# Kernel optimization log

Measured on AMD Instinct MI355X. Metric: run time of the kernel, lower is better.

## Reference

```python
import jax, jax.numpy as jnp
import numpy as np

EPS = 1e-5
QMAX = 127.0   # 8-bit symmetric: representable range [-128, 127]
QMIN = -128.0


def ste_round(x):
    # straight-through rounding (identity gradient)
    return x + jax.lax.stop_gradient(jnp.round(x) - x)


def setup_inputs() -> dict:
    key = jax.random.key(0)
    ks = jax.random.split(key, 7)
    N, C_in, C_out, H, W = 64, 256, 128, 56, 56
    x = jax.random.normal(ks[0], (N, C_in, H, W), jnp.float32)
    act_scaling_factor = jax.random.uniform(ks[1], (1,), jnp.float32, 0.02, 0.08)
    bn_weight = 1.0 + 0.3 * jax.random.normal(ks[2], (C_in,), jnp.float32)
    bn_bias = 0.1 * jax.random.normal(ks[3], (C_in,), jnp.float32)
    bn_mean = 0.1 * jax.random.normal(ks[4], (C_in,), jnp.float32)
    bn_var = jax.random.uniform(ks[5], (C_in,), jnp.float32, 0.5, 1.5)
    conv_weight = 0.05 * jax.random.normal(ks[6], (C_out, C_in, 1, 1), jnp.float32)
    return {
        "x": x,
        "act_scaling_factor": act_scaling_factor,
        "bn_weight": bn_weight,
        "bn_bias": bn_bias,
        "bn_mean": bn_mean,
        "bn_var": bn_var,
        "conv_weight": conv_weight,
    }


def _fwd(x, act_scaling_factor, bn_weight, bn_bias, bn_mean, bn_var, conv_weight):
    act_sf = act_scaling_factor.reshape(())

    # ---- QuantBn: fold BN, quantize folded scale per-channel (8-bit symmetric) ----
    inv_std = jax.lax.rsqrt(bn_var + EPS)
    scale = bn_weight * inv_std                    # [C_in]
    shift = bn_bias - bn_mean * scale              # [C_in]
    bn_sf = jnp.max(jnp.abs(scale)) / QMAX         # per-tensor bn weight scale
    scale_q = jnp.clip(ste_round(scale / bn_sf), QMIN, QMAX) * bn_sf
    bias_sf = bn_sf * act_sf                        # bias quantized at combined scale
    shift_q = ste_round(shift / bias_sf) * bias_sf
    x = x * scale_q[None, :, None, None] + shift_q[None, :, None, None]

    # ---- ReLU ----
    x = jnp.maximum(x, 0.0)

    # ---- QuantAct 1: per-tensor symmetric 8-bit requant ----
    sf1 = jnp.max(jnp.abs(x)) / QMAX
    x = jnp.clip(ste_round(x / sf1), QMIN, QMAX) * sf1

    # ---- QuantConv2d: per-output-channel 8-bit symmetric weight quant, 1x1 conv ----
    w_sf = jnp.max(jnp.abs(conv_weight), axis=(1, 2, 3)) / QMAX   # [C_out]
    w_q = jnp.clip(ste_round(conv_weight / w_sf[:, None, None, None]), QMIN, QMAX) \
          * w_sf[:, None, None, None]
    y = jax.lax.conv_general_dilated(
        x, w_q, window_strides=(1, 1), padding='VALID',
        dimension_numbers=('NCHW', 'OIHW', 'NCHW'))

    # ---- QuantAct 2 ----
    sf2 = jnp.max(jnp.abs(y)) / QMAX
    y = jnp.clip(ste_round(y / sf2), QMIN, QMAX) * sf2

    # ---- QuantAveragePool2d (2x2, stride 2): average in integer domain, re-round ----
    N, C, H, W = y.shape
    y_int = (y / sf2).reshape(N, C, H // 2, 2, W // 2, 2).mean(axis=(3, 5))
    out = ste_round(y_int) * sf2
    return out, sf2


def reference(x, act_scaling_factor, bn_weight, bn_bias, bn_mean, bn_var, conv_weight):
    return _fwd(x, act_scaling_factor, bn_weight, bn_bias, bn_mean, bn_var, conv_weight)
```

## Files before the change

kernel.cpp:

```cpp
#include <hip/hip_runtime.h>

#define QMAXF 127.0f
typedef int i32x4 __attribute__((ext_vector_type(4)));

__device__ __forceinline__ unsigned fkey(float f) {
  const unsigned b = __float_as_uint(f);
  return (b & 0x80000000u) ? ~b : (b | 0x80000000u);
}
__device__ __forceinline__ float fdec(unsigned u) {
  return __uint_as_float((u & 0x80000000u) ? (u & 0x7FFFFFFFu) : ~u);
}

__global__ __launch_bounds__(256) void k0_zero(unsigned* __restrict__ p) {
  const int t = threadIdx.x;
  p[t] = 0u; p[t + 256] = 0u; p[t + 512] = 0u; p[t + 768] = 0u;
}

__global__ __launch_bounds__(256, 8) void k1_minmax(
    const float* __restrict__ x, const float* __restrict__ actsf,
    const float* __restrict__ bnw, const float* __restrict__ bnb,
    const float* __restrict__ bnm, const float* __restrict__ bnv,
    const float* __restrict__ cw, unsigned* __restrict__ chanKmx,
    unsigned* __restrict__ chanKmn, float* __restrict__ scq,
    float* __restrict__ shq, float* __restrict__ wsf,
    signed char* __restrict__ wq8) {
  const int t = threadIdx.x, b = blockIdx.x;
  if (b == 2048) {
    __shared__ float red[4];
    float scale, shift;
    {
#pragma clang fp contract(off)
      float inv = 1.0f / sqrtf(bnv[t] + 1e-5f);
      scale = bnw[t] * inv;
      float tmp = bnm[t] * scale;
      shift = bnb[t] - tmp;
    }
    float a = fabsf(scale);
    for (int o = 32; o > 0; o >>= 1) a = fmaxf(a, __shfl_xor(a, o));
    if ((t & 63) == 0) red[t >> 6] = a;
    __syncthreads();
    const float amax = fmaxf(fmaxf(red[0], red[1]), fmaxf(red[2], red[3]));
    const float bn_sf = amax / QMAXF;
    scq[t] = fminf(fmaxf(rintf(scale / bn_sf), -128.f), 127.f) * bn_sf;
    const float bias_sf = bn_sf * actsf[0];
    shq[t] = rintf(shift / bias_sf) * bias_sf;
    const int r = t >> 1, half = t & 1;
    const float4* wrow = (const float4*)(cw + r * 256 + half * 128);
    float mx = 0.f;
#pragma unroll
    for (int j = 0; j < 32; ++j) {
      const float4 v = wrow[j];
      mx = fmaxf(mx, fmaxf(fmaxf(fabsf(v.x), fabsf(v.y)), fmaxf(fabsf(v.z), fabsf(v.w))));
    }
    mx = fmaxf(mx, __shfl_xor(mx, 1));
    const float wsf_v = mx / QMAXF;
    if (half == 0) wsf[r] = wsf_v;
    int* w8w = (int*)wq8;
#pragma unroll
    for (int j = 0; j < 32; ++j) {
      const float4 v = wrow[j];
      const float q0 = fminf(fmaxf(rintf(v.x / wsf_v), -128.f), 127.f);
      const float q1 = fminf(fmaxf(rintf(v.y / wsf_v), -128.f), 127.f);
      const float q2 = fminf(fmaxf(rintf(v.z / wsf_v), -128.f), 127.f);
      const float q3 = fminf(fmaxf(rintf(v.w / wsf_v), -128.f), 127.f);
      w8w[r * 64 + half * 32 + j] =
          ((int)q0 & 255) | (((int)q1 & 255) << 8) | (((int)q2 & 255) << 16) | (((int)q3 & 255) << 24);
    }
    return;
  }
  __shared__ float redmn[4][8], redmx[4][8];
  const int n = b >> 5, cg = b & 31;
  const float4* __restrict__ x4 = (const float4*)x + (long)(n * 256 + cg * 8) * 784;
  float mn[8], mx[8];
#pragma unroll
  for (int r = 0; r < 8; ++r) { mn[r] = __builtin_inff(); mx[r] = -__builtin_inff(); }
#pragma unroll
  for (int r = 0; r < 8; ++r) {
    const float4* row = x4 + r * 784;
    for (int j = t; j < 784; j += 256) {
      const float4 v = row[j];
      mn[r] = fminf(mn[r], fminf(fminf(v.x, v.y), fminf(v.z, v.w)));
      mx[r] = fmaxf(mx[r], fmaxf(fmaxf(v.x, v.y), fmaxf(v.z, v.w)));
    }
  }
#pragma unroll
  for (int r = 0; r < 8; ++r)
    for (int o = 32; o > 0; o >>= 1) {
      mn[r] = fminf(mn[r], __shfl_xor(mn[r], o));
      mx[r] = fmaxf(mx[r], __shfl_xor(mx[r], o));
    }
  if ((t & 63) == 0) {
#pragma unroll
    for (int r = 0; r < 8; ++r) { redmn[t >> 6][r] = mn[r]; redmx[t >> 6][r] = mx[r]; }
  }
  __syncthreads();
  if (t < 8) {
    const float fmn = fminf(fminf(redmn[0][t], redmn[1][t]), fminf(redmn[2][t], redmn[3][t]));
    const float fmx = fmaxf(fmaxf(redmx[0][t], redmx[1][t]), fmaxf(redmx[2][t], redmx[3][t]));
    atomicMax(&chanKmx[cg * 8 + t], fkey(fmx));
    atomicMax(&chanKmn[cg * 8 + t], ~fkey(fmn));
  }
}

__global__ __launch_bounds__(256, 4) void k2f_quant_gemm(
    const float* __restrict__ x, const float* __restrict__ scq,
    const float* __restrict__ shq, const unsigned* __restrict__ chanKmx,
    const unsigned* __restrict__ chanKmn, const signed char* __restrict__ wq8,
    const float* __restrict__ wsf, signed char* __restrict__ xqT,
    float* __restrict__ blockmax) {
  __shared__ __align__(16) unsigned char ldsb[112 * 256];
  __shared__ float s_scq[256], s_shq[256];
  __shared__ float comax[128];
  __shared__ float red[4];
  __shared__ float sf1s;
  const int t = threadIdx.x, w = t >> 6, l = t & 63, m = l & 15, g = l >> 4;
  const int blk = blockIdx.x, n = blk / 28, tt = blk - n * 28;

  {
    const float s = scq[t], sh = shq[t];
    s_scq[t] = s; s_shq[t] = sh;
    const float xe = (s >= 0.f) ? fdec(chanKmx[t]) : fdec(~chanKmn[t]);
    float z;
    {
#pragma clang fp contract(off)
      z = xe * s + sh;
    }
    float mm = fmaxf(z, 0.f);
    for (int o = 32; o > 0; o >>= 1) mm = fmaxf(mm, __shfl_xor(mm, o));
    if (l == 0) red[w] = mm;
    __syncthreads();
    if (t == 0) sf1s = fmaxf(fmaxf(red[0], red[1]), fmaxf(red[2], red[3])) / QMAXF;
    __syncthreads();
  }
  const float sf1 = sf1s;
  const float* __restrict__ xb = x + (long)n * 802816 + tt * 112;

  for (int it = 0; it < 28; ++it) {
    const int idx = it * 256 + t;
    const int c = idx / 28;
    const int p = idx - c * 28;
    const float4 v = *(const float4*)(xb + (long)c * 3136 + 4 * p);
    const float s = s_scq[c], sh = s_shq[c];
    float z0, z1, z2, z3;
    {
#pragma clang fp contract(off)
      z0 = v.x * s + sh; z1 = v.y * s + sh; z2 = v.z * s + sh; z3 = v.w * s + sh;
    }
    const float q0 = fminf(fmaxf(rintf(fmaxf(z0, 0.f) / sf1), -128.f), 127.f);
    const float q1 = fminf(fmaxf(rintf(fmaxf(z1, 0.f) / sf1), -128.f), 127.f);
    const float q2 = fminf(fmaxf(rintf(fmaxf(z2, 0.f) / sf1), -128.f), 127.f);
    const float q3 = fminf(fmaxf(rintf(fmaxf(z3, 0.f) / sf1), -128.f), 127.f);
    const int cs = c ^ ((p & 15) << 4);
    const int hw0 = 4 * p;
    ldsb[(hw0 + 0) * 256 + cs] = (unsigned char)((int)q0 & 255);
    ldsb[(hw0 + 1) * 256 + cs] = (unsigned char)((int)q1 & 255);
    ldsb[(hw0 + 2) * 256 + cs] = (unsigned char)((int)q2 & 255);
    ldsb[(hw0 + 3) * 256 + cs] = (unsigned char)((int)q3 & 255);
  }
  __syncthreads();

  signed char* __restrict__ dst = xqT + ((long)(n * 3136 + tt * 112)) * 256;
#pragma unroll
  for (int it = 0; it < 7; ++it) {
    const int idx = it * 256 + t;
    const int hw = idx >> 4, c16 = idx & 15;
    const i32x4 v = *(const i32x4*)&ldsb[hw * 256 + ((c16 * 16) ^ (((hw >> 2) & 15) << 4))];
    *(i32x4*)(dst + hw * 256 + c16 * 16) = v;
  }

  i32x4 acc[2][7];
#pragma unroll
  for (int ct = 0; ct < 2; ++ct)
#pragma unroll
    for (int ht = 0; ht < 7; ++ht) acc[ct][ht] = (i32x4){0, 0, 0, 0};
#pragma unroll
  for (int ks = 0; ks < 4; ++ks) {
    const i32x4 wf0 = *(const i32x4*)(wq8 + (w * 32 + m) * 256 + ks * 64 + g * 16);
    const i32x4 wf1 = *(const i32x4*)(wq8 + (w * 32 + 16 + m) * 256 + ks * 64 + g * 16);
#pragma unroll
    for (int ht = 0; ht < 7; ++ht) {
      const int row = ht * 16 + m;
      const i32x4 xf = *(const i32x4*)&ldsb[row * 256 +
                          ((ks * 64 + g * 16) ^ (((row >> 2) & 15) << 4))];
      acc[0][ht] = __builtin_amdgcn_mfma_i32_16x16x64_i8(wf0, xf, acc[0][ht], 0, 0, 0);
      acc[1][ht] = __builtin_amdgcn_mfma_i32_16x16x64_i8(wf1, xf, acc[1][ht], 0, 0, 0);
    }
  }

  int im[2][4];
#pragma unroll
  for (int ct = 0; ct < 2; ++ct)
#pragma unroll
    for (int r = 0; r < 4; ++r) {
      int v = 0;
#pragma unroll
      for (int ht = 0; ht < 7; ++ht) {
        int a = acc[ct][ht][r];
        a = a < 0 ? -a : a;
        v = a > v ? a : v;
      }
      im[ct][r] = v;
    }
#pragma unroll
  for (int o = 1; o < 16; o <<= 1)
#pragma unroll
    for (int ct = 0; ct < 2; ++ct)
#pragma unroll
      for (int r = 0; r < 4; ++r) {
        const int other = __shfl_xor(im[ct][r], o);
        im[ct][r] = other > im[ct][r] ? other : im[ct][r];
      }
  if (m == 0) {
#pragma unroll
    for (int ct = 0; ct < 2; ++ct)
#pragma unroll
      for (int r = 0; r < 4; ++r)
        comax[w * 32 + ct * 16 + g * 4 + r] = (float)im[ct][r];
  }
  __syncthreads();
  float v = 0.f;
  if (t < 128) v = comax[t] * (sf1 * wsf[t]);
  for (int o = 32; o > 0; o >>= 1) v = fmaxf(v, __shfl_xor(v, o));
  if (l == 0) red[w] = v;
  __syncthreads();
  if (t == 0)
    blockmax[blk] = fmaxf(fmaxf(red[0], red[1]), fmaxf(red[2], red[3]));
}

__global__ __launch_bounds__(256, 3) void k3_final(
    const signed char* __restrict__ xqT, const signed char* __restrict__ wq8,
    const float* __restrict__ wsf, const float* __restrict__ scq,
    const float* __restrict__ shq, const unsigned* __restrict__ chanKmx,
    const unsigned* __restrict__ chanKmn, const float* __restrict__ blockmax,
    float* __restrict__ out, float* __restrict__ outsf2) {
  __shared__ _Float16 q2[128 * 116];
  __shared__ float red[4];
  __shared__ float sf1s, sf2s;
  const int t = threadIdx.x, w = t >> 6, l = t & 63;
  const int m = l & 15, g = l >> 4;
  const int blk = blockIdx.x;
  const int n = blk / 28, tt = blk - n * 28;

  {
    const float s = scq[t], sh = shq[t];
    const float xe = (s >= 0.f) ? fdec(chanKmx[t]) : fdec(~chanKmn[t]);
    float z;
    {
#pragma clang fp contract(off)
      z = xe * s + sh;
    }
    float mm = fmaxf(z, 0.f);
    for (int o = 32; o > 0; o >>= 1) mm = fmaxf(mm, __shfl_xor(mm, o));
    if (l == 0) red[w] = mm;
    __syncthreads();
    if (t == 0) sf1s = fmaxf(fmaxf(red[0], red[1]), fmaxf(red[2], red[3])) / QMAXF;
  }
  {
    float bm = 0.f;
    for (int i = t; i < 1792; i += 256) bm = fmaxf(bm, blockmax[i]);
    for (int o = 32; o > 0; o >>= 1) bm = fmaxf(bm, __shfl_xor(bm, o));
    __syncthreads();
    if (l == 0) red[w] = bm;
    __syncthreads();
    if (t == 0) sf2s = fmaxf(fmaxf(red[0], red[1]), fmaxf(red[2], red[3])) / QMAXF;
    __syncthreads();
  }
  const float sf1 = sf1s;
  const float sf2 = sf2s;
  if (blk == 0 && t == 0) outsf2[0] = sf2;

  const signed char* __restrict__ xb = xqT + ((long)(n * 3136 + tt * 112)) * 256;
  i32x4 acc[2][7];
#pragma unroll
  for (int ct = 0; ct < 2; ++ct)
#pragma unroll
    for (int ht = 0; ht < 7; ++ht) acc[ct][ht] = (i32x4){0, 0, 0, 0};
#pragma unroll
  for (int ks = 0; ks < 4; ++ks) {
    const i32x4 wf0 = *(const i32x4*)(wq8 + (w * 32 + m) * 256 + ks * 64 + g * 16);
    const i32x4 wf1 = *(const i32x4*)(wq8 + (w * 32 + 16 + m) * 256 + ks * 64 + g * 16);
#pragma unroll
    for (int ht = 0; ht < 7; ++ht) {
      const i32x4 xf = *(const i32x4*)(xb + (ht * 16 + m) * 256 + ks * 64 + g * 16);
      acc[0][ht] = __builtin_amdgcn_mfma_i32_16x16x64_i8(wf0, xf, acc[0][ht], 0, 0, 0);
      acc[1][ht] = __builtin_amdgcn_mfma_i32_16x16x64_i8(wf1, xf, acc[1][ht], 0, 0, 0);
    }
  }
  float fac[2][4];
#pragma unroll
  for (int ct = 0; ct < 2; ++ct)
#pragma unroll
    for (int r = 0; r < 4; ++r)
      fac[ct][r] = sf1 * wsf[w * 32 + ct * 16 + g * 4 + r];
#pragma unroll
  for (int ct = 0; ct < 2; ++ct)
#pragma unroll
    for (int ht = 0; ht < 7; ++ht)
#pragma unroll
      for (int r = 0; r < 4; ++r) {
        const float y = (float)acc[ct][ht][r] * fac[ct][r];
        const float q = fminf(fmaxf(rintf(y / sf2), -128.f), 127.f);
        q2[(w * 32 + ct * 16 + g * 4 + r) * 116 + ht * 16 + m] = (_Float16)q;
      }
  __syncthreads();
  const long obase = (long)n * 100352 + tt * 28;
  for (int i = t; i < 3584; i += 256) {
    const unsigned co = (unsigned)i / 28u;
    const unsigned wo = (unsigned)i - co * 28u;
    const _Float16* row = q2 + co * 116;
    const float a = (float)row[2 * wo] + (float)row[2 * wo + 1] +
                    (float)row[56 + 2 * wo] + (float)row[56 + 2 * wo + 1];
    out[obase + (long)co * 784 + wo] = rintf(a * 0.25f) * sf2;
  }
}

extern "C" void kernel_launch(void* const* d_in, const int* in_sizes, int n_in,
                              void* d_out, int out_size, void* d_ws, size_t ws_size,
                              hipStream_t stream) {
  const float* x     = (const float*)d_in[0];
  const float* actsf = (const float*)d_in[1];
  const float* bnw   = (const float*)d_in[2];
  const float* bnb   = (const float*)d_in[3];
  const float* bnm   = (const float*)d_in[4];
  const float* bnv   = (const float*)d_in[5];
  const float* cw    = (const float*)d_in[6];
  float* out = (float*)d_out;
  char* ws = (char*)d_ws;

  unsigned* chanKmx   = (unsigned*)(ws + 256);
  unsigned* chanKmn   = (unsigned*)(ws + 1280);
  float* scq          = (float*)(ws + 4096);
  float* shq          = (float*)(ws + 5120);
  float* wsf          = (float*)(ws + 6144);
  signed char* wq8    = (signed char*)(ws + 8192);
  float* blockmax     = (float*)(ws + 40960);
  signed char* xqT    = (signed char*)(ws + 65536);
  float* outsf2       = out + (out_size - 1);

  hipLaunchKernelGGL(k0_zero, dim3(1), dim3(256), 0, stream, (unsigned*)ws);
  hipLaunchKernelGGL(k1_minmax, dim3(2049), dim3(256), 0, stream,
                     x, actsf, bnw, bnb, bnm, bnv, cw, chanKmx, chanKmn, scq, shq, wsf, wq8);
  hipLaunchKernelGGL(k2f_quant_gemm, dim3(1792), dim3(256), 0, stream,
                     x, scq, shq, chanKmx, chanKmn, wq8, wsf, xqT, blockmax);
  hipLaunchKernelGGL(k3_final, dim3(1792), dim3(256), 0, stream,
                     xqT, wq8, wsf, scq, shq, chanKmx, chanKmn, blockmax, out, outsf2);
}
```

Measured before the change: 151.6 us.

## Store int32 GEMM results instead of recomputing GEMM in final kernel

The quant-GEMM kernel no longer writes the transposed int8 activations. Instead it stages its int32 accumulators through shared memory and writes them to a global y32 buffer. The final kernel becomes a simple elementwise pool kernel: it reads y32, requantizes with sf2, does the 2x2 average and writes the output, so the second MFMA GEMM pass is gone. The cost is an int32 intermediate that is four times the size of the int8 activations it replaces, which roughly doubles global memory traffic between the two kernels and needs a much larger workspace.

```diff
diff --git a/kernel.cpp b/kernel.cpp
--- a/kernel.cpp
+++ b/kernel.cpp
@@ -102,13 +102,18 @@
   }
 }
 
+union K2Lds {
+  unsigned char b[112 * 256];
+  int w[64 * 116];
+};
+
 __global__ __launch_bounds__(256, 4) void k2f_quant_gemm(
     const float* __restrict__ x, const float* __restrict__ scq,
     const float* __restrict__ shq, const unsigned* __restrict__ chanKmx,
     const unsigned* __restrict__ chanKmn, const signed char* __restrict__ wq8,
-    const float* __restrict__ wsf, signed char* __restrict__ xqT,
+    const float* __restrict__ wsf, int* __restrict__ y32,
     float* __restrict__ blockmax) {
-  __shared__ __align__(16) unsigned char ldsb[112 * 256];
+  __shared__ K2Lds lds;
   __shared__ float s_scq[256], s_shq[256];
   __shared__ float comax[128];
   __shared__ float red[4];
@@ -152,21 +157,12 @@
     const float q3 = fminf(fmaxf(rintf(fmaxf(z3, 0.f) / sf1), -128.f), 127.f);
     const int cs = c ^ ((p & 15) << 4);
     const int hw0 = 4 * p;
-    ldsb[(hw0 + 0) * 256 + cs] = (unsigned char)((int)q0 & 255);
-    ldsb[(hw0 + 1) * 256 + cs] = (unsigned char)((int)q1 & 255);
-    ldsb[(hw0 + 2) * 256 + cs] = (unsigned char)((int)q2 & 255);
-    ldsb[(hw0 + 3) * 256 + cs] = (unsigned char)((int)q3 & 255);
-  }
-  __syncthreads();
-
-  signed char* __restrict__ dst = xqT + ((long)(n * 3136 + tt * 112)) * 256;
-#pragma unroll
-  for (int it = 0; it < 7; ++it) {
-    const int idx = it * 256 + t;
-    const int hw = idx >> 4, c16 = idx & 15;
-    const i32x4 v = *(const i32x4*)&ldsb[hw * 256 + ((c16 * 16) ^ (((hw >> 2) & 15) << 4))];
-    *(i32x4*)(dst + hw * 256 + c16 * 16) = v;
-  }
+    lds.b[(hw0 + 0) * 256 + cs] = (unsigned char)((int)q0 & 255);
+    lds.b[(hw0 + 1) * 256 + cs] = (unsigned char)((int)q1 & 255);
+    lds.b[(hw0 + 2) * 256 + cs] = (unsigned char)((int)q2 & 255);
+    lds.b[(hw0 + 3) * 256 + cs] = (unsigned char)((int)q3 & 255);
+  }
+  __syncthreads();
 
   i32x4 acc[2][7];
 #pragma unroll
@@ -180,10 +176,28 @@
 #pragma unroll
     for (int ht = 0; ht < 7; ++ht) {
       const int row = ht * 16 + m;
-      const i32x4 xf = *(const i32x4*)&ldsb[row * 256 +
+      const i32x4 xf = *(const i32x4*)&lds.b[row * 256 +
                           ((ks * 64 + g * 16) ^ (((row >> 2) & 15) << 4))];
       acc[0][ht] = __builtin_amdgcn_mfma_i32_16x16x64_i8(wf0, xf, acc[0][ht], 0, 0, 0);
       acc[1][ht] = __builtin_amdgcn_mfma_i32_16x16x64_i8(wf1, xf, acc[1][ht], 0, 0, 0);
+    }
+  }
+
+  for (int ct = 0; ct < 2; ++ct) {
+    __syncthreads();
+    const int co_l = w * 16 + g * 4;
+#pragma unroll
+    for (int ht = 0; ht < 7; ++ht)
+#pragma unroll
+      for (int r = 0; r < 4; ++r)
+        lds.w[(co_l + r) * 116 + ht * 16 + m] = acc[ct][ht][r];
+    __syncthreads();
+    for (int it = 0; it < 28; ++it) {
+      const int i = it * 256 + t;
+      const int cl = i / 112;
+      const int pos = i - cl * 112;
+      const int co = ((cl >> 4) << 5) + ct * 16 + (cl & 15);
+      y32[((long)(n * 128 + co)) * 3136 + tt * 112 + pos] = lds.w[cl * 116 + pos];
     }
   }
 
@@ -210,6 +224,7 @@
         const int other = __shfl_xor(im[ct][r], o);
         im[ct][r] = other > im[ct][r] ? other : im[ct][r];
       }
+  __syncthreads();
   if (m == 0) {
 #pragma unroll
     for (int ct = 0; ct < 2; ++ct)
@@ -227,19 +242,16 @@
     blockmax[blk] = fmaxf(fmaxf(red[0], red[1]), fmaxf(red[2], red[3]));
 }
 
-__global__ __launch_bounds__(256, 3) void k3_final(
-    const signed char* __restrict__ xqT, const signed char* __restrict__ wq8,
-    const float* __restrict__ wsf, const float* __restrict__ scq,
-    const float* __restrict__ shq, const unsigned* __restrict__ chanKmx,
-    const unsigned* __restrict__ chanKmn, const float* __restrict__ blockmax,
-    float* __restrict__ out, float* __restrict__ outsf2) {
-  __shared__ _Float16 q2[128 * 116];
+__global__ __launch_bounds__(256, 8) void k3_pool(
+    const int* __restrict__ y32, const float* __restrict__ wsf,
+    const float* __restrict__ scq, const float* __restrict__ shq,
+    const unsigned* __restrict__ chanKmx, const unsigned* __restrict__ chanKmn,
+    const float* __restrict__ blockmax, float* __restrict__ out,
+    float* __restrict__ outsf2) {
   __shared__ float red[4];
   __shared__ float sf1s, sf2s;
   const int t = threadIdx.x, w = t >> 6, l = t & 63;
-  const int m = l & 15, g = l >> 4;
-  const int blk = blockIdx.x;
-  const int n = blk / 28, tt = blk - n * 28;
+  const int b = blockIdx.x;
 
   {
     const float s = scq[t], sh = shq[t];
@@ -267,50 +279,27 @@
   }
   const float sf1 = sf1s;
   const float sf2 = sf2s;
-  if (blk == 0 && t == 0) outsf2[0] = sf2;
-
-  const signed char* __restrict__ xb = xqT + ((long)(n * 3136 + tt * 112)) * 256;
-  i32x4 acc[2][7];
-#pragma unroll
-  for (int ct = 0; ct < 2; ++ct)
-#pragma unroll
-    for (int ht = 0; ht < 7; ++ht) acc[ct][ht] = (i32x4){0, 0, 0, 0};
-#pragma unroll
-  for (int ks = 0; ks < 4; ++ks) {
-    const i32x4 wf0 = *(const i32x4*)(wq8 + (w * 32 + m) * 256 + ks * 64 + g * 16);
-    const i32x4 wf1 = *(const i32x4*)(wq8 + (w * 32 + 16 + m) * 256 + ks * 64 + g * 16);
-#pragma unroll
-    for (int ht = 0; ht < 7; ++ht) {
-      const i32x4 xf = *(const i32x4*)(xb + (ht * 16 + m) * 256 + ks * 64 + g * 16);
-      acc[0][ht] = __builtin_amdgcn_mfma_i32_16x16x64_i8(wf0, xf, acc[0][ht], 0, 0, 0);
-      acc[1][ht] = __builtin_amdgcn_mfma_i32_16x16x64_i8(wf1, xf, acc[1][ht], 0, 0, 0);
-    }
-  }
-  float fac[2][4];
-#pragma unroll
-  for (int ct = 0; ct < 2; ++ct)
-#pragma unroll
-    for (int r = 0; r < 4; ++r)
-      fac[ct][r] = sf1 * wsf[w * 32 + ct * 16 + g * 4 + r];
-#pragma unroll
-  for (int ct = 0; ct < 2; ++ct)
-#pragma unroll
-    for (int ht = 0; ht < 7; ++ht)
-#pragma unroll
-      for (int r = 0; r < 4; ++r) {
-        const float y = (float)acc[ct][ht][r] * fac[ct][r];
-        const float q = fminf(fmaxf(rintf(y / sf2), -128.f), 127.f);
-        q2[(w * 32 + ct * 16 + g * 4 + r) * 116 + ht * 16 + m] = (_Float16)q;
-      }
-  __syncthreads();
-  const long obase = (long)n * 100352 + tt * 28;
-  for (int i = t; i < 3584; i += 256) {
-    const unsigned co = (unsigned)i / 28u;
-    const unsigned wo = (unsigned)i - co * 28u;
-    const _Float16* row = q2 + co * 116;
-    const float a = (float)row[2 * wo] + (float)row[2 * wo + 1] +
-                    (float)row[56 + 2 * wo] + (float)row[56 + 2 * wo + 1];
-    out[obase + (long)co * 784 + wo] = rintf(a * 0.25f) * sf2;
+  if (b == 0 && t == 0) outsf2[0] = sf2;
+
+#pragma unroll
+  for (int k = 0; k < 14; ++k) {
+    const int idx = b * 256 + t + k * 458752;
+    const int n = idx / 100352;
+    const int rem = idx - n * 100352;
+    const int co = rem / 784;
+    const int j = rem - co * 784;
+    const int ho = j / 28;
+    const int wo = j - ho * 28;
+    const long rowb = ((long)(n * 128 + co)) * 3136 + ho * 112 + 2 * wo;
+    const int2 a = *(const int2*)(y32 + rowb);
+    const int2 c = *(const int2*)(y32 + rowb + 56);
+    const float fac = sf1 * wsf[co];
+    const float q0 = fminf(fmaxf(rintf(((float)a.x * fac) / sf2), -128.f), 127.f);
+    const float q1 = fminf(fmaxf(rintf(((float)a.y * fac) / sf2), -128.f), 127.f);
+    const float q2 = fminf(fmaxf(rintf(((float)c.x * fac) / sf2), -128.f), 127.f);
+    const float q3 = fminf(fmaxf(rintf(((float)c.y * fac) / sf2), -128.f), 127.f);
+    const float s4 = q0 + q1 + q2 + q3;
+    out[idx] = rintf(s4 * 0.25f) * sf2;
   }
 }
 
@@ -334,14 +323,14 @@
   float* wsf          = (float*)(ws + 6144);
   signed char* wq8    = (signed char*)(ws + 8192);
   float* blockmax     = (float*)(ws + 40960);
-  signed char* xqT    = (signed char*)(ws + 65536);
+  int* y32            = (int*)(ws + 65536);
   float* outsf2       = out + (out_size - 1);
 
   hipLaunchKernelGGL(k0_zero, dim3(1), dim3(256), 0, stream, (unsigned*)ws);
   hipLaunchKernelGGL(k1_minmax, dim3(2049), dim3(256), 0, stream,
                      x, actsf, bnw, bnb, bnm, bnv, cw, chanKmx, chanKmn, scq, shq, wsf, wq8);
   hipLaunchKernelGGL(k2f_quant_gemm, dim3(1792), dim3(256), 0, stream,
-                     x, scq, shq, chanKmx, chanKmn, wq8, wsf, xqT, blockmax);
-  hipLaunchKernelGGL(k3_final, dim3(1792), dim3(256), 0, stream,
-                     xqT, wq8, wsf, scq, shq, chanKmx, chanKmn, blockmax, out, outsf2);
-}
+                     x, scq, shq, chanKmx, chanKmn, wq8, wsf, y32, blockmax);
+  hipLaunchKernelGGL(k3_pool, dim3(1792), dim3(256), 0, stream,
+                     y32, wsf, scq, shq, chanKmx, chanKmn, blockmax, out, outsf2);
+}
```

Measured after the change: 167.3 us. 10.4% more time.

## Replace atomic channel min/max with per-batch partials and pack int8 LDS writes

Applied to the files above, without the earlier changes.

The per-channel min/max reduction no longer uses atomicMax on order-preserving float keys. Each block now writes its result to a per-(channel, batch) partial array, so the zeroing kernel launch can be dropped. The consumer kernels reduce the 64 partials per channel in a shared preamble. The quantize stage in k2f also gathers four channels per thread and packs them into 32-bit words before storing to LDS, replacing byte-wide LDS stores. The trade-off is extra global reads of partials in every block of k2f and k3.

```diff
diff --git a/kernel.cpp b/kernel.cpp
--- a/kernel.cpp
+++ b/kernel.cpp
@@ -2,26 +2,13 @@
 
 #define QMAXF 127.0f
 typedef int i32x4 __attribute__((ext_vector_type(4)));
-
-__device__ __forceinline__ unsigned fkey(float f) {
-  const unsigned b = __float_as_uint(f);
-  return (b & 0x80000000u) ? ~b : (b | 0x80000000u);
-}
-__device__ __forceinline__ float fdec(unsigned u) {
-  return __uint_as_float((u & 0x80000000u) ? (u & 0x7FFFFFFFu) : ~u);
-}
-
-__global__ __launch_bounds__(256) void k0_zero(unsigned* __restrict__ p) {
-  const int t = threadIdx.x;
-  p[t] = 0u; p[t + 256] = 0u; p[t + 512] = 0u; p[t + 768] = 0u;
-}
 
 __global__ __launch_bounds__(256, 8) void k1_minmax(
     const float* __restrict__ x, const float* __restrict__ actsf,
     const float* __restrict__ bnw, const float* __restrict__ bnb,
     const float* __restrict__ bnm, const float* __restrict__ bnv,
-    const float* __restrict__ cw, unsigned* __restrict__ chanKmx,
-    unsigned* __restrict__ chanKmn, float* __restrict__ scq,
+    const float* __restrict__ cw, float* __restrict__ partmx,
+    float* __restrict__ partmn, float* __restrict__ scq,
     float* __restrict__ shq, float* __restrict__ wsf,
     signed char* __restrict__ wq8) {
   const int t = threadIdx.x, b = blockIdx.x;
@@ -97,18 +84,50 @@
   if (t < 8) {
     const float fmn = fminf(fminf(redmn[0][t], redmn[1][t]), fminf(redmn[2][t], redmn[3][t]));
     const float fmx = fmaxf(fmaxf(redmx[0][t], redmx[1][t]), fmaxf(redmx[2][t], redmx[3][t]));
-    atomicMax(&chanKmx[cg * 8 + t], fkey(fmx));
-    atomicMax(&chanKmn[cg * 8 + t], ~fkey(fmn));
-  }
+    partmx[(cg * 8 + t) * 64 + n] = fmx;
+    partmn[(cg * 8 + t) * 64 + n] = fmn;
+  }
+}
+
+__device__ __forceinline__ float sf1_preamble(
+    const float* __restrict__ scq, const float* __restrict__ shq,
+    const float* __restrict__ partmx, const float* __restrict__ partmn,
+    float* s_scq, float* s_shq, float* red, float* sf1s) {
+  const int t = threadIdx.x, w = t >> 6, l = t & 63;
+  const float s = scq[t], sh = shq[t];
+  if (s_scq) { s_scq[t] = s; s_shq[t] = sh; }
+  const float4* pm = (const float4*)(partmx + t * 64);
+  const float4* pn = (const float4*)(partmn + t * 64);
+  float xmx = -__builtin_inff(), xmn = __builtin_inff();
+#pragma unroll
+  for (int j = 0; j < 16; ++j) {
+    const float4 a = pm[j];
+    xmx = fmaxf(xmx, fmaxf(fmaxf(a.x, a.y), fmaxf(a.z, a.w)));
+    const float4 bq = pn[j];
+    xmn = fminf(xmn, fminf(fminf(bq.x, bq.y), fminf(bq.z, bq.w)));
+  }
+  const float xe = (s >= 0.f) ? xmx : xmn;
+  float z;
+  {
+#pragma clang fp contract(off)
+    z = xe * s + sh;
+  }
+  float mm = fmaxf(z, 0.f);
+  for (int o = 32; o > 0; o >>= 1) mm = fmaxf(mm, __shfl_xor(mm, o));
+  if (l == 0) red[w] = mm;
+  __syncthreads();
+  if (t == 0) *sf1s = fmaxf(fmaxf(red[0], red[1]), fmaxf(red[2], red[3])) / QMAXF;
+  __syncthreads();
+  return *sf1s;
 }
 
 __global__ __launch_bounds__(256, 4) void k2f_quant_gemm(
     const float* __restrict__ x, const float* __restrict__ scq,
-    const float* __restrict__ shq, const unsigned* __restrict__ chanKmx,
-    const unsigned* __restrict__ chanKmn, const signed char* __restrict__ wq8,
+    const float* __restrict__ shq, const float* __restrict__ partmx,
+    const float* __restrict__ partmn, const signed char* __restrict__ wq8,
     const float* __restrict__ wsf, signed char* __restrict__ xqT,
     float* __restrict__ blockmax) {
-  __shared__ __align__(16) unsigned char ldsb[112 * 256];
+  __shared__ __align__(16) int wlds[112 * 64];
   __shared__ float s_scq[256], s_shq[256];
   __shared__ float comax[128];
   __shared__ float red[4];
@@ -116,46 +135,37 @@
   const int t = threadIdx.x, w = t >> 6, l = t & 63, m = l & 15, g = l >> 4;
   const int blk = blockIdx.x, n = blk / 28, tt = blk - n * 28;
 
-  {
-    const float s = scq[t], sh = shq[t];
-    s_scq[t] = s; s_shq[t] = sh;
-    const float xe = (s >= 0.f) ? fdec(chanKmx[t]) : fdec(~chanKmn[t]);
-    float z;
-    {
+  const float sf1 = sf1_preamble(scq, shq, partmx, partmn, s_scq, s_shq, red, &sf1s);
+  const float* __restrict__ xb = x + (long)n * 802816 + tt * 112;
+
+  for (int it = 0; it < 7; ++it) {
+    const int task = it * 256 + t;
+    const int cq = task / 28;
+    const int p = task - cq * 28;
+    const int hw0 = 4 * p;
+    int wds[4] = {0, 0, 0, 0};
+#pragma unroll
+    for (int j = 0; j < 4; ++j) {
+      const int c = 4 * cq + j;
+      const float4 v = *(const float4*)(xb + (long)c * 3136 + hw0);
+      const float s = s_scq[c], sh = s_shq[c];
+      float z0, z1, z2, z3;
+      {
 #pragma clang fp contract(off)
-      z = xe * s + sh;
-    }
-    float mm = fmaxf(z, 0.f);
-    for (int o = 32; o > 0; o >>= 1) mm = fmaxf(mm, __shfl_xor(mm, o));
-    if (l == 0) red[w] = mm;
-    __syncthreads();
-    if (t == 0) sf1s = fmaxf(fmaxf(red[0], red[1]), fmaxf(red[2], red[3])) / QMAXF;
-    __syncthreads();
-  }
-  const float sf1 = sf1s;
-  const float* __restrict__ xb = x + (long)n * 802816 + tt * 112;
-
-  for (int it = 0; it < 28; ++it) {
-    const int idx = it * 256 + t;
-    const int c = idx / 28;
-    const int p = idx - c * 28;
-    const float4 v = *(const float4*)(xb + (long)c * 3136 + 4 * p);
-    const float s = s_scq[c], sh = s_shq[c];
-    float z0, z1, z2, z3;
-    {
-#pragma clang fp contract(off)
-      z0 = v.x * s + sh; z1 = v.y * s + sh; z2 = v.z * s + sh; z3 = v.w * s + sh;
-    }
-    const float q0 = fminf(fmaxf(rintf(fmaxf(z0, 0.f) / sf1), -128.f), 127.f);
-    const float q1 = fminf(fmaxf(rintf(fmaxf(z1, 0.f) / sf1), -128.f), 127.f);
-    const float q2 = fminf(fmaxf(rintf(fmaxf(z2, 0.f) / sf1), -128.f), 127.f);
-    const float q3 = fminf(fmaxf(rintf(fmaxf(z3, 0.f) / sf1), -128.f), 127.f);
-    const int cs = c ^ ((p & 15) << 4);
-    const int hw0 = 4 * p;
-    ldsb[(hw0 + 0) * 256 + cs] = (unsigned char)((int)q0 & 255);
-    ldsb[(hw0 + 1) * 256 + cs] = (unsigned char)((int)q1 & 255);
-    ldsb[(hw0 + 2) * 256 + cs] = (unsigned char)((int)q2 & 255);
-    ldsb[(hw0 + 3) * 256 + cs] = (unsigned char)((int)q3 & 255);
+        z0 = v.x * s + sh; z1 = v.y * s + sh; z2 = v.z * s + sh; z3 = v.w * s + sh;
+      }
+      const float q0 = fminf(fmaxf(rintf(fmaxf(z0, 0.f) / sf1), -128.f), 127.f);
+      const float q1 = fminf(fmaxf(rintf(fmaxf(z1, 0.f) / sf1), -128.f), 127.f);
+      const float q2 = fminf(fmaxf(rintf(fmaxf(z2, 0.f) / sf1), -128.f), 127.f);
+      const float q3 = fminf(fmaxf(rintf(fmaxf(z3, 0.f) / sf1), -128.f), 127.f);
+      wds[0] |= ((int)q0 & 255) << (8 * j);
+      wds[1] |= ((int)q1 & 255) << (8 * j);
+      wds[2] |= ((int)q2 & 255) << (8 * j);
+      wds[3] |= ((int)q3 & 255) << (8 * j);
+    }
+    const int col = cq ^ ((p & 15) << 2);
+#pragma unroll
+    for (int d = 0; d < 4; ++d) wlds[(hw0 + d) * 64 + col] = wds[d];
   }
   __syncthreads();
 
@@ -164,7 +174,7 @@
   for (int it = 0; it < 7; ++it) {
     const int idx = it * 256 + t;
     const int hw = idx >> 4, c16 = idx & 15;
-    const i32x4 v = *(const i32x4*)&ldsb[hw * 256 + ((c16 * 16) ^ (((hw >> 2) & 15) << 4))];
+    const i32x4 v = *(const i32x4*)&wlds[hw * 64 + ((c16 * 4) ^ (((hw >> 2) & 15) << 2))];
     *(i32x4*)(dst + hw * 256 + c16 * 16) = v;
   }
 
@@ -180,8 +190,8 @@
 #pragma unroll
     for (int ht = 0; ht < 7; ++ht) {
       const int row = ht * 16 + m;
-      const i32x4 xf = *(const i32x4*)&ldsb[row * 256 +
-                          ((ks * 64 + g * 16) ^ (((row >> 2) & 15) << 4))];
+      const i32x4 xf = *(const i32x4*)&wlds[row * 64 +
+                          ((ks * 16 + g * 4) ^ (((row >> 2) & 15) << 2))];
       acc[0][ht] = __builtin_amdgcn_mfma_i32_16x16x64_i8(wf0, xf, acc[0][ht], 0, 0, 0);
       acc[1][ht] = __builtin_amdgcn_mfma_i32_16x16x64_i8(wf1, xf, acc[1][ht], 0, 0, 0);
     }
@@ -230,8 +240,8 @@
 __global__ __launch_bounds__(256, 3) void k3_final(
     const signed char* __restrict__ xqT, const signed char* __restrict__ wq8,
     const float* __restrict__ wsf, const float* __restrict__ scq,
-    const float* __restrict__ shq, const unsigned* __restrict__ chanKmx,
-    const unsigned* __restrict__ chanKmn, const float* __restrict__ blockmax,
+    const float* __restrict__ shq, const float* __restrict__ partmx,
+    const float* __restrict__ partmn, const float* __restrict__ blockmax,
     float* __restrict__ out, float* __restrict__ outsf2) {
   __shared__ _Float16 q2[128 * 116];
   __shared__ float red[4];
@@ -241,20 +251,7 @@
   const int blk = blockIdx.x;
   const int n = blk / 28, tt = blk - n * 28;
 
-  {
-    const float s = scq[t], sh = shq[t];
-    const float xe = (s >= 0.f) ? fdec(chanKmx[t]) : fdec(~chanKmn[t]);
-    float z;
-    {
-#pragma clang fp contract(off)
-      z = xe * s + sh;
-    }
-    float mm = fmaxf(z, 0.f);
-    for (int o = 32; o > 0; o >>= 1) mm = fmaxf(mm, __shfl_xor(mm, o));
-    if (l == 0) red[w] = mm;
-    __syncthreads();
-    if (t == 0) sf1s = fmaxf(fmaxf(red[0], red[1]), fmaxf(red[2], red[3])) / QMAXF;
-  }
+  const float sf1 = sf1_preamble(scq, shq, partmx, partmn, nullptr, nullptr, red, &sf1s);
   {
     float bm = 0.f;
     for (int i = t; i < 1792; i += 256) bm = fmaxf(bm, blockmax[i]);
@@ -265,7 +262,6 @@
     if (t == 0) sf2s = fmaxf(fmaxf(red[0], red[1]), fmaxf(red[2], red[3])) / QMAXF;
     __syncthreads();
   }
-  const float sf1 = sf1s;
   const float sf2 = sf2s;
   if (blk == 0 && t == 0) outsf2[0] = sf2;
 
@@ -327,21 +323,20 @@
   float* out = (float*)d_out;
   char* ws = (char*)d_ws;
 
-  unsigned* chanKmx   = (unsigned*)(ws + 256);
-  unsigned* chanKmn   = (unsigned*)(ws + 1280);
-  float* scq          = (float*)(ws + 4096);
-  float* shq          = (float*)(ws + 5120);
-  float* wsf          = (float*)(ws + 6144);
-  signed char* wq8    = (signed char*)(ws + 8192);
-  float* blockmax     = (float*)(ws + 40960);
-  signed char* xqT    = (signed char*)(ws + 65536);
+  float* scq          = (float*)(ws);
+  float* shq          = (float*)(ws + 1024);
+  float* wsf          = (float*)(ws + 2048);
+  float* partmx       = (float*)(ws + 4096);
+  float* partmn       = (float*)(ws + 69632);
+  signed char* wq8    = (signed char*)(ws + 135168);
+  float* blockmax     = (float*)(ws + 167936);
+  signed char* xqT    = (signed char*)(ws + 262144);
   float* outsf2       = out + (out_size - 1);
 
-  hipLaunchKernelGGL(k0_zero, dim3(1), dim3(256), 0, stream, (unsigned*)ws);
   hipLaunchKernelGGL(k1_minmax, dim3(2049), dim3(256), 0, stream,
-                     x, actsf, bnw, bnb, bnm, bnv, cw, chanKmx, chanKmn, scq, shq, wsf, wq8);
+                     x, actsf, bnw, bnb, bnm, bnv, cw, partmx, partmn, scq, shq, wsf, wq8);
   hipLaunchKernelGGL(k2f_quant_gemm, dim3(1792), dim3(256), 0, stream,
-                     x, scq, shq, chanKmx, chanKmn, wq8, wsf, xqT, blockmax);
+                     x, scq, shq, partmx, partmn, wq8, wsf, xqT, blockmax);
   hipLaunchKernelGGL(k3_final, dim3(1792), dim3(256), 0, stream,
-                     xqT, wq8, wsf, scq, shq, chanKmx, chanKmn, blockmax, out, outsf2);
-}
+                     xqT, wq8, wsf, scq, shq, partmx, partmn, blockmax, out, outsf2);
+}
```

Result: slower. 180.0 us (+18.7%).
